# Performance work log

Measured on AMD Instinct MI355X. Metric: run time of the kernel, lower is better.

## Reference

```python
import jax, jax.numpy as jnp
import numpy as np

B_, L_, DM_, DS_, DC_, EXP_ = 2, 2048, 1024, 16, 4, 2
DI_ = EXP_ * DM_

def setup_inputs() -> dict:
    key = jax.random.key(0)
    ks = jax.random.split(key, 8)
    rn = lambda k, shape, s: (jax.random.normal(k, shape, dtype=jnp.float32) * s)
    return {
        "x": rn(ks[0], (B_, L_, DM_), 1.0),
        "in_proj_w": rn(ks[1], (2 * DI_, DM_), 0.02),
        "conv_w": rn(ks[2], (DI_, 1, DC_), 0.1),
        "conv_b": jnp.zeros((DI_,), dtype=jnp.float32),
        "x_proj_w": rn(ks[3], (2 * DS_ + 1, DI_), 0.02),
        "dt_proj_w": rn(ks[4], (DI_, 1), 0.02),
        "dt_proj_b": jnp.full((DI_,), -2.0, dtype=jnp.float32),
        "A_log": rn(ks[5], (DI_, DS_), 1.0),
        "D": jnp.ones((DI_,), dtype=jnp.float32),
        "out_proj_w": rn(ks[6], (DM_, DI_), 0.02),
    }


def reference(x, in_proj_w, conv_w, conv_b, x_proj_w, dt_proj_w, dt_proj_b, A_log, D, out_proj_w):
    b, l, dm = x.shape
    di, ds = A_log.shape
    dc = conv_w.shape[-1]

    # in_proj -> split into u (ssm stream) and z (gate)
    xz = x @ in_proj_w.T                      # (b, l, 2*di)
    u, z = xz[..., :di], xz[..., di:]

    # causal depthwise conv1d (torch pads both sides then slices [:l] == left pad only)
    uc = jnp.transpose(u, (0, 2, 1))          # (b, di, l)
    uc = jax.lax.conv_general_dilated(
        uc, conv_w, window_strides=(1,), padding=[(dc - 1, 0)],
        feature_group_count=di, dimension_numbers=("NCH", "OIH", "NCH"))
    uc = uc + conv_b[None, :, None]
    u = jnp.transpose(uc, (0, 2, 1)) * jax.nn.silu(z)   # (b, l, di)

    # input-dependent SSM params
    proj = u @ x_proj_w.T                     # (b, l, 2*ds + 1)
    delta = proj[..., :1]                     # (b, l, 1)
    Bm = proj[..., 1:1 + ds]                  # (b, l, ds)
    Cm = proj[..., 1 + ds:]                   # (b, l, ds)
    delta = jax.nn.softplus(delta @ dt_proj_w.T + dt_proj_b)  # (b, l, di)

    A = -jnp.exp(A_log)                       # (di, ds)

    def step(h, inp):
        ut, dt, Bt, Ct = inp                  # (b,di) (b,di) (b,ds) (b,ds)
        dte = jnp.exp(dt)                     # faithful to source: exp(softplus(...))
        A_bar = jnp.exp(A[None] * dte[..., None])          # (b, di, ds)
        h = A_bar * h + (Bt[:, None, :] * dte[..., None]) * ut[..., None]
        yt = jnp.einsum("bis,bs->bi", h, Ct) + D * ut
        return h, yt

    h0 = jnp.zeros((b, di, ds), dtype=x.dtype)
    xs = (jnp.transpose(u, (1, 0, 2)), jnp.transpose(delta, (1, 0, 2)),
          jnp.transpose(Bm, (1, 0, 2)), jnp.transpose(Cm, (1, 0, 2)))
    _, ys = jax.lax.scan(step, h0, xs)        # ys: (l, b, di)
    y = jnp.transpose(ys, (1, 0, 2))          # (b, l, di)
    return y @ out_proj_w.T                   # (b, l, dm)
```

## Files before the change

kernel.cpp:

```cpp
#include <hip/hip_runtime.h>
#include <hip/hip_bf16.h>
#include <cstddef>
#include <cstdint>

#define B_N 2
#define L_N 2048
#define DM_N 1024
#define DS_N 16
#define DI_N 2048
#define NTOK (B_N * L_N)
#define NPROJ 33
#define NPJ 36
#define NC 64
#define CL (L_N / NC)
#define XKC 8
#define XKCL (DI_N / XKC)

typedef __attribute__((ext_vector_type(8))) short short8v;
typedef __attribute__((ext_vector_type(4))) float f32x4;
typedef __attribute__((address_space(1))) void av1;
typedef __attribute__((address_space(3))) void av3;

__device__ __forceinline__ void gload16(const void* g, void* l) {
  __builtin_amdgcn_global_load_lds((av1*)g, (av3*)l, 16, 0, 0);
}

__device__ __forceinline__ unsigned short f2bf_rn(float f) {
  uint32_t u = __float_as_uint(f);
  uint32_t r = (u + 0x7fffu + ((u >> 16) & 1u)) >> 16;
  return (unsigned short)r;
}
__device__ __forceinline__ float bf2f(unsigned short h) {
  return __uint_as_float((uint32_t)h << 16);
}

__global__ __launch_bounds__(256) void split_pack_kernel(
    const float* __restrict__ src, uint32_t* __restrict__ dst, int n8) {
  int idx = blockIdx.x * 256 + threadIdx.x;
  if (idx >= n8) return;
  const float4* s = (const float4*)src + (size_t)idx * 2;
  float4 v0 = s[0], v1 = s[1];
  float f[8] = {v0.x, v0.y, v0.z, v0.w, v1.x, v1.y, v1.z, v1.w};
  uint32_t hi[4], lo[4];
#pragma unroll
  for (int j = 0; j < 4; ++j) {
    unsigned short h0 = f2bf_rn(f[2 * j]);
    unsigned short h1 = f2bf_rn(f[2 * j + 1]);
    unsigned short l0 = f2bf_rn(f[2 * j] - bf2f(h0));
    unsigned short l1 = f2bf_rn(f[2 * j + 1] - bf2f(h1));
    hi[j] = (uint32_t)h0 | ((uint32_t)h1 << 16);
    lo[j] = (uint32_t)l0 | ((uint32_t)l1 << 16);
  }
  uint4* d = (uint4*)dst + (size_t)idx * 2;
  d[0] = make_uint4(hi[0], hi[1], hi[2], hi[3]);
  d[1] = make_uint4(lo[0], lo[1], lo[2], lo[3]);
}

__global__ __launch_bounds__(256) void gemm_pk_nt(
    const char* __restrict__ Apk, const char* __restrict__ Bpk,
    float* __restrict__ C, int N, int K4, int gx) {
  __shared__ __align__(16) char lds[32768];
  const int tid = threadIdx.x;
  const int lane = tid & 63;
  const int wave = tid >> 6;

  const int nwg = gridDim.x;
  const int cpx = nwg >> 3;
  const int bid = blockIdx.x;
  const int wg = (bid & 7) * cpx + (bid >> 3);
  const int bx = wg % gx;
  const int by = wg / gx;
  const int m0 = by * 128, n0 = bx * 128;

  const int wr = wave >> 1, wc = wave & 1;

  const char* gbase = (wave & 2) ? Bpk : Apk;
  const int rowbase = ((wave & 2) ? n0 : m0) + (wave & 1) * 64;
  const int rloc = lane >> 3;
  const int sslot = (lane & 7) ^ rloc;
  const char* gsrc = gbase + (size_t)(rowbase + rloc) * K4 + sslot * 16;
  const size_t cstride = (size_t)8 * K4;
  char* ldst = lds + wave * 8192 + lane * 16;

  f32x4 acc[4][4] = {};
  const int fr = lane & 15;
  const int fg = lane >> 4;
  const int sA = ((fg * 2) ^ (fr & 7)) * 16;
  const int abase = (wr * 64 + fr) * 128 + sA;
  const int bbase = 16384 + (wc * 64 + fr) * 128 + sA;

  for (int kt4 = 0; kt4 < K4; kt4 += 128) {
#pragma unroll
    for (int c = 0; c < 8; ++c)
      gload16(gsrc + c * cstride + kt4, ldst + c * 1024);
    __syncthreads();

    short8v afh[4], afl[4], bfh[4], bfl[4];
#pragma unroll
    for (int m = 0; m < 4; ++m) {
      int a = abase + m * 2048;
      afh[m] = *(const short8v*)(lds + a);
      afl[m] = *(const short8v*)(lds + (a ^ 16));
    }
#pragma unroll
    for (int n = 0; n < 4; ++n) {
      int b = bbase + n * 2048;
      bfh[n] = *(const short8v*)(lds + b);
      bfl[n] = *(const short8v*)(lds + (b ^ 16));
    }
#pragma unroll
    for (int m = 0; m < 4; ++m) {
#pragma unroll
      for (int n = 0; n < 4; ++n) {
        asm("v_mfma_f32_16x16x32_bf16 %0, %1, %2, %0"
            : "+v"(acc[m][n]) : "v"(afh[m]), "v"(bfh[n]));
        asm("v_mfma_f32_16x16x32_bf16 %0, %1, %2, %0"
            : "+v"(acc[m][n]) : "v"(afh[m]), "v"(bfl[n]));
        asm("v_mfma_f32_16x16x32_bf16 %0, %1, %2, %0"
            : "+v"(acc[m][n]) : "v"(afl[m]), "v"(bfh[n]));
      }
    }
    __syncthreads();
  }

#pragma unroll
  for (int m = 0; m < 4; ++m) {
#pragma unroll
    for (int n = 0; n < 4; ++n) {
#pragma unroll
      for (int q = 0; q < 4; ++q) {
        int row = m0 + wr * 64 + m * 16 + fg * 4 + q;
        int col = n0 + wc * 64 + n * 16 + fr;
        C[(size_t)row * N + col] = acc[m][n][q];
      }
    }
  }
}

__global__ __launch_bounds__(256) void gemm2_pk_nt(
    const char* __restrict__ Apk, const char* __restrict__ Bpk,
    float* __restrict__ C) {
  __shared__ __align__(16) char lds[24576];
  const int tid = threadIdx.x;
  const int lane = tid & 63;
  const int wave = tid >> 6;
  const int K4 = DI_N * 4;

  const int bid = blockIdx.x;
  const int wg = (bid & 7) * 64 + (bid >> 3);
  const int bx = wg >> 6;
  const int by = wg & 63;
  const int m0 = by * 64, n0 = bx * 128;

  const int rloc = tid >> 3;
  const int sl = (tid & 7) ^ (rloc & 7);
  const char* gA = Apk + (size_t)(m0 + rloc) * K4 + sl * 16;
  const char* gB = Bpk + (size_t)(n0 + rloc) * K4 + sl * 16;
  const size_t cs = (size_t)32 * K4;
  char* ldst = lds + tid * 16;

  f32x4 acc[4][2] = {};
  const int fr = lane & 15;
  const int fg = lane >> 4;
  const int sA = ((fg * 2) ^ (fr & 7)) * 16;
  const int abase0 = fr * 128 + sA;
  const int bbase0 = 8192 + (wave * 32 + fr) * 128 + sA;

  for (int kt4 = 0; kt4 < K4; kt4 += 128) {
    gload16(gA + kt4, ldst);
    gload16(gA + cs + kt4, ldst + 4096);
    gload16(gB + kt4, ldst + 8192);
    gload16(gB + cs + kt4, ldst + 12288);
    gload16(gB + 2 * cs + kt4, ldst + 16384);
    gload16(gB + 3 * cs + kt4, ldst + 20480);
    __syncthreads();

    short8v afh[4], afl[4], bfh[2], bfl[2];
#pragma unroll
    for (int m = 0; m < 4; ++m) {
      int a = abase0 + m * 2048;
      afh[m] = *(const short8v*)(lds + a);
      afl[m] = *(const short8v*)(lds + (a ^ 16));
    }
#pragma unroll
    for (int n = 0; n < 2; ++n) {
      int b = bbase0 + n * 2048;
      bfh[n] = *(const short8v*)(lds + b);
      bfl[n] = *(const short8v*)(lds + (b ^ 16));
    }
#pragma unroll
    for (int m = 0; m < 4; ++m) {
#pragma unroll
      for (int n = 0; n < 2; ++n) {
        asm("v_mfma_f32_16x16x32_bf16 %0, %1, %2, %0"
            : "+v"(acc[m][n]) : "v"(afh[m]), "v"(bfh[n]));
        asm("v_mfma_f32_16x16x32_bf16 %0, %1, %2, %0"
            : "+v"(acc[m][n]) : "v"(afh[m]), "v"(bfl[n]));
        asm("v_mfma_f32_16x16x32_bf16 %0, %1, %2, %0"
            : "+v"(acc[m][n]) : "v"(afl[m]), "v"(bfh[n]));
      }
    }
    __syncthreads();
  }

#pragma unroll
  for (int m = 0; m < 4; ++m) {
#pragma unroll
    for (int n = 0; n < 2; ++n) {
#pragma unroll
      for (int q = 0; q < 4; ++q) {
        int row = m0 + m * 16 + fg * 4 + q;
        int col = n0 + wave * 32 + n * 16 + fr;
        C[(size_t)row * DM_N + col] = acc[m][n][q];
      }
    }
  }
}

__global__ __launch_bounds__(256) void conv_silu_kernel(
    const float* __restrict__ xz, const float* __restrict__ cw,
    const float* __restrict__ cb, float* __restrict__ u2) {
  int idx = blockIdx.x * 256 + threadIdx.x;
  int i4 = idx & (DI_N / 4 - 1);
  int n = idx >> 9;
  int i = i4 << 2;
  int l = n & (L_N - 1);
  const float* base = xz + (size_t)n * (2 * DI_N) + i;
  float4 zero = {0.f, 0.f, 0.f, 0.f};
  float4 u0 = *(const float4*)base;
  float4 u1 = (l >= 1) ? *(const float4*)(base - 2 * DI_N) : zero;
  float4 um2 = (l >= 2) ? *(const float4*)(base - 4 * DI_N) : zero;
  float4 um3 = (l >= 3) ? *(const float4*)(base - 6 * DI_N) : zero;
  float4 z = *(const float4*)(base + DI_N);
  float4 bia = *(const float4*)&cb[i];
  float4 w0 = *(const float4*)&cw[i * 4];
  float4 w1 = *(const float4*)&cw[i * 4 + 4];
  float4 w2 = *(const float4*)&cw[i * 4 + 8];
  float4 w3 = *(const float4*)&cw[i * 4 + 12];
  float4 r;
  r.x = fmaf(w0.w, u0.x, fmaf(w0.z, u1.x, fmaf(w0.y, um2.x, fmaf(w0.x, um3.x, bia.x))));
  r.y = fmaf(w1.w, u0.y, fmaf(w1.z, u1.y, fmaf(w1.y, um2.y, fmaf(w1.x, um3.y, bia.y))));
  r.z = fmaf(w2.w, u0.z, fmaf(w2.z, u1.z, fmaf(w2.y, um2.z, fmaf(w2.x, um3.z, bia.z))));
  r.w = fmaf(w3.w, u0.w, fmaf(w3.z, u1.w, fmaf(w3.y, um2.w, fmaf(w3.x, um3.w, bia.w))));
  r.x *= z.x / (1.f + __expf(-z.x));
  r.y *= z.y / (1.f + __expf(-z.y));
  r.z *= z.z / (1.f + __expf(-z.z));
  r.w *= z.w / (1.f + __expf(-z.w));
  *(float4*)&u2[(size_t)n * DI_N + i] = r;
}

__global__ __launch_bounds__(256) void xproj_part_kernel(
    const float* __restrict__ u2, const float* __restrict__ xw,
    float* __restrict__ part) {
  __shared__ float uS[16][257];
  __shared__ float wS[33][257];
  const int tid = threadIdx.x;
  const int kc = blockIdx.x & (XKC - 1);
  const int rb = blockIdx.x >> 3;
  const int row0 = rb * 16;
  const int k0 = kc * XKCL;

#pragma unroll
  for (int it = 0; it < 4; ++it) {
    int slot = tid + it * 256;
    int r = slot >> 6;
    int kq = (slot & 63) << 2;
    float4 v = *(const float4*)&u2[(size_t)(row0 + r) * DI_N + k0 + kq];
    uS[r][kq] = v.x; uS[r][kq + 1] = v.y;
    uS[r][kq + 2] = v.z; uS[r][kq + 3] = v.w;
  }
#pragma unroll
  for (int it = 0; it < 9; ++it) {
    int slot = tid + it * 256;
    if (slot < 33 * 64) {
      int c = slot >> 6;
      int kq = (slot & 63) << 2;
      float4 v = *(const float4*)&xw[(size_t)c * DI_N + k0 + kq];
      wS[c][kq] = v.x; wS[c][kq + 1] = v.y;
      wS[c][kq + 2] = v.z; wS[c][kq + 3] = v.w;
    }
  }
  __syncthreads();

  const int r = tid & 15;
  const int cg = tid >> 4;
  const int c0 = cg * 3;
  const int rc0 = c0 > 32 ? 32 : c0;
  const int rc1 = c0 + 1 > 32 ? 32 : c0 + 1;
  const int rc2 = c0 + 2 > 32 ? 32 : c0 + 2;
  float a0 = 0.f, a1 = 0.f, a2 = 0.f;
#pragma unroll 4
  for (int k = 0; k < XKCL; ++k) {
    float uv = uS[r][k];
    a0 = fmaf(uv, wS[rc0][k], a0);
    a1 = fmaf(uv, wS[rc1][k], a1);
    a2 = fmaf(uv, wS[rc2][k], a2);
  }
  size_t base = (size_t)kc * (NTOK * NPJ) + (size_t)(row0 + r) * NPJ;
  if (c0 < NPROJ)     part[base + (c0 == 0 ? 0 : c0 + 3)] = a0;
  if (c0 + 1 < NPROJ) part[base + c0 + 4] = a1;
  if (c0 + 2 < NPROJ) part[base + c0 + 5] = a2;
  if (cg == 11) {
    part[base + 1] = 0.f; part[base + 2] = 0.f; part[base + 3] = 0.f;
  }
}

__global__ __launch_bounds__(256) void xproj_reduce_kernel(
    const float* __restrict__ part, float* __restrict__ proj) {
  int idx = blockIdx.x * 256 + threadIdx.x;
  float s = 0.f;
#pragma unroll
  for (int kc = 0; kc < XKC; ++kc)
    s += part[(size_t)kc * (NTOK * NPJ) + idx];
  proj[idx] = s;
}

__global__ __launch_bounds__(256) void scan_pass1_kernel(
    const float* __restrict__ u2, const float* __restrict__ pj,
    const float* __restrict__ dtw, const float* __restrict__ dtb,
    const float* __restrict__ A_log,
    float* __restrict__ carryH, float* __restrict__ sdteO) {
  __shared__ float pS[CL][20];
  const int tid = threadIdx.x;
  const int bid = blockIdx.x;
  const int ib = bid & 7;
  const int c = (bid >> 3) & (NC - 1);
  const int b = bid >> 9;
  const int i = ib * 256 + tid;
  const int l0 = c * CL;
  const float LOG2E = 1.4426950408889634f;

  if (tid < CL * 5) {
    int row = tid / 5, j = tid % 5;
    float4 v = *(const float4*)&pj[((size_t)b * L_N + l0 + row) * NPJ + j * 4];
    *(float4*)&pS[row][j * 4] = v;
  }

  float A2[16];
#pragma unroll
  for (int q = 0; q < 4; ++q) {
    float4 v = *(const float4*)&A_log[i * DS_N + q * 4];
    A2[q * 4 + 0] = -__expf(v.x) * LOG2E;
    A2[q * 4 + 1] = -__expf(v.y) * LOG2E;
    A2[q * 4 + 2] = -__expf(v.z) * LOG2E;
    A2[q * 4 + 3] = -__expf(v.w) * LOG2E;
  }
  const float wl = dtw[i] * LOG2E;
  const float bl = dtb[i] * LOG2E;
  const float* un = u2 + ((size_t)b * L_N + l0) * DI_N + i;
  __syncthreads();

  float h[16] = {};
  float sdte = 0.f;
  float ucur = un[0];
#pragma unroll 2
  for (int l = 0; l < CL; ++l) {
    float unext = (l + 1 < CL) ? un[(size_t)(l + 1) * DI_N] : 0.f;
    float d0 = pS[l][0];
    float4 B0 = *(const float4*)&pS[l][4];
    float4 B1 = *(const float4*)&pS[l][8];
    float4 B2 = *(const float4*)&pS[l][12];
    float4 B3 = *(const float4*)&pS[l][16];
    float dte = 1.f + exp2f(fmaf(d0, wl, bl));
    float du = dte * ucur;
    sdte += dte;
    float Bv[16] = {B0.x, B0.y, B0.z, B0.w, B1.x, B1.y, B1.z, B1.w,
                    B2.x, B2.y, B2.z, B2.w, B3.x, B3.y, B3.z, B3.w};
#pragma unroll
    for (int s = 0; s < 16; ++s) {
      float a = exp2f(A2[s] * dte);
      h[s] = fmaf(a, h[s], Bv[s] * du);
    }
    ucur = unext;
  }
  size_t cbase = (((size_t)c * B_N + b) * DI_N + i) * DS_N;
#pragma unroll
  for (int q = 0; q < 4; ++q) {
    float4 hv = {h[q * 4], h[q * 4 + 1], h[q * 4 + 2], h[q * 4 + 3]};
    *(float4*)&carryH[cbase + q * 4] = hv;
  }
  sdteO[((size_t)c * B_N + b) * DI_N + i] = sdte;
}

__global__ __launch_bounds__(256) void scan_fixup_kernel(
    float* __restrict__ carryH, const float* __restrict__ sdte,
    const float* __restrict__ A_log) {
  const int q = blockIdx.x * 256 + threadIdx.x;
  const int s = q & 15;
  const int i = (q >> 4) & (DI_N - 1);
  const float LOG2E = 1.4426950408889634f;
  const float A2 = -__expf(A_log[i * DS_N + s]) * LOG2E;
  float h = 0.f;
#pragma unroll 8
  for (int c = 0; c < NC; ++c) {
    size_t idx = (size_t)c * (B_N * DI_N * DS_N) + q;
    float Hc = carryH[idx];
    float sd = sdte[(size_t)c * (B_N * DI_N) + (q >> 4)];
    carryH[idx] = h;
    h = fmaf(exp2f(A2 * sd), h, Hc);
  }
}

__global__ __launch_bounds__(256) void scan_pass2_kernel(
    const float* __restrict__ u2, const float* __restrict__ pj,
    const float* __restrict__ dtw, const float* __restrict__ dtb,
    const float* __restrict__ A_log, const float* __restrict__ Dp,
    const float* __restrict__ carryH, char* __restrict__ ypk) {
  __shared__ float pS[CL][36];
  const int tid = threadIdx.x;
  const int bid = blockIdx.x;
  const int ib = bid & 7;
  const int c = (bid >> 3) & (NC - 1);
  const int b = bid >> 9;
  const int i = ib * 256 + tid;
  const int l0 = c * CL;
  const float LOG2E = 1.4426950408889634f;

#pragma unroll
  for (int it = 0; it < 2; ++it) {
    int slot = tid + it * 256;
    if (slot < CL * 9) {
      int row = slot / 9, j = slot % 9;
      float4 v = *(const float4*)&pj[((size_t)b * L_N + l0 + row) * NPJ + j * 4];
      *(float4*)&pS[row][j * 4] = v;
    }
  }

  float A2[16];
#pragma unroll
  for (int q = 0; q < 4; ++q) {
    float4 v = *(const float4*)&A_log[i * DS_N + q * 4];
    A2[q * 4 + 0] = -__expf(v.x) * LOG2E;
    A2[q * 4 + 1] = -__expf(v.y) * LOG2E;
    A2[q * 4 + 2] = -__expf(v.z) * LOG2E;
    A2[q * 4 + 3] = -__expf(v.w) * LOG2E;
  }
  const float wl = dtw[i] * LOG2E;
  const float bl = dtb[i] * LOG2E;
  const float Dd = Dp[i];

  float h[16];
  size_t cbase = (((size_t)c * B_N + b) * DI_N + i) * DS_N;
#pragma unroll
  for (int q = 0; q < 4; ++q) {
    float4 hv = *(const float4*)&carryH[cbase + q * 4];
    h[q * 4] = hv.x; h[q * 4 + 1] = hv.y;
    h[q * 4 + 2] = hv.z; h[q * 4 + 3] = hv.w;
  }

  const float* un = u2 + ((size_t)b * L_N + l0) * DI_N + i;
  char* yb = ypk + ((size_t)b * L_N + l0) * (DI_N * 4) + (i >> 3) * 32 + (i & 7) * 2;
  __syncthreads();

  float ucur = un[0];
#pragma unroll 2
  for (int l = 0; l < CL; ++l) {
    float unext = (l + 1 < CL) ? un[(size_t)(l + 1) * DI_N] : 0.f;
    float d0 = pS[l][0];
    float4 B0 = *(const float4*)&pS[l][4];
    float4 B1 = *(const float4*)&pS[l][8];
    float4 B2 = *(const float4*)&pS[l][12];
    float4 B3 = *(const float4*)&pS[l][16];
    float4 C0 = *(const float4*)&pS[l][20];
    float4 C1 = *(const float4*)&pS[l][24];
    float4 C2 = *(const float4*)&pS[l][28];
    float4 C3 = *(const float4*)&pS[l][32];
    float dte = 1.f + exp2f(fmaf(d0, wl, bl));
    float du = dte * ucur;
    float Bv[16] = {B0.x, B0.y, B0.z, B0.w, B1.x, B1.y, B1.z, B1.w,
                    B2.x, B2.y, B2.z, B2.w, B3.x, B3.y, B3.z, B3.w};
    float Cv[16] = {C0.x, C0.y, C0.z, C0.w, C1.x, C1.y, C1.z, C1.w,
                    C2.x, C2.y, C2.z, C2.w, C3.x, C3.y, C3.z, C3.w};
    float y = Dd * ucur;
#pragma unroll
    for (int s = 0; s < 16; ++s) {
      float a = exp2f(A2[s] * dte);
      h[s] = fmaf(a, h[s], Bv[s] * du);
      y = fmaf(h[s], Cv[s], y);
    }
    unsigned short hh = f2bf_rn(y);
    char* q = yb + (size_t)l * (DI_N * 4);
    *(unsigned short*)q = hh;
    *(unsigned short*)(q + 16) = f2bf_rn(y - bf2f(hh));
    ucur = unext;
  }
}

extern "C" void kernel_launch(void* const* d_in, const int* in_sizes, int n_in,
                              void* d_out, int out_size, void* d_ws, size_t ws_size,
                              hipStream_t stream) {
  const float* x          = (const float*)d_in[0];
  const float* in_proj_w  = (const float*)d_in[1];
  const float* conv_w     = (const float*)d_in[2];
  const float* conv_b     = (const float*)d_in[3];
  const float* x_proj_w   = (const float*)d_in[4];
  const float* dt_proj_w  = (const float*)d_in[5];
  const float* dt_proj_b  = (const float*)d_in[6];
  const float* A_log      = (const float*)d_in[7];
  const float* Dp         = (const float*)d_in[8];
  const float* out_proj_w = (const float*)d_in[9];
  float* out = (float*)d_out;

  char* ws = (char*)d_ws;
  float* xz = (float*)ws;
  float* u2 = (float*)(ws + (size_t)NTOK * 2 * DI_N * 4);

  char* x_pk  = (char*)u2;
  char* w1_pk = x_pk + (size_t)NTOK * DM_N * 4;

  char*  y_pk   = ws;
  float* carryH = (float*)(ws + 33554432);
  float* sdte   = (float*)(ws + 50331648);
  char*  w2_pk  = ws + 51380224;
  float* xpart  = (float*)(ws + 59768832);
  float* proj36 = (float*)(ws + 64487424);

  {
    int n8 = NTOK * DM_N / 8;
    split_pack_kernel<<<n8 / 256, 256, 0, stream>>>(x, (uint32_t*)x_pk, n8);
    split_pack_kernel<<<n8 / 256, 256, 0, stream>>>(in_proj_w, (uint32_t*)w1_pk, n8);
  }
  gemm_pk_nt<<<1024, 256, 0, stream>>>(x_pk, w1_pk, xz, 2 * DI_N, DM_N * 4, 32);
  conv_silu_kernel<<<(NTOK * DI_N / 4) / 256, 256, 0, stream>>>(xz, conv_w,
                                                                conv_b, u2);
  {
    int n8 = DM_N * DI_N / 8;
    split_pack_kernel<<<n8 / 256, 256, 0, stream>>>(out_proj_w, (uint32_t*)w2_pk, n8);
  }
  {
    xproj_part_kernel<<<(NTOK / 16) * XKC, 256, 0, stream>>>(u2, x_proj_w, xpart);
    xproj_reduce_kernel<<<(NTOK * NPJ) / 256, 256, 0, stream>>>(xpart, proj36);
  }
  {
    int nblk = B_N * NC * (DI_N / 256);
    scan_pass1_kernel<<<nblk, 256, 0, stream>>>(u2, proj36, dt_proj_w, dt_proj_b,
                                                A_log, carryH, sdte);
    scan_fixup_kernel<<<(B_N * DI_N * DS_N) / 256, 256, 0, stream>>>(carryH, sdte,
                                                                     A_log);
    scan_pass2_kernel<<<nblk, 256, 0, stream>>>(u2, proj36, dt_proj_w, dt_proj_b,
                                                A_log, Dp, carryH, y_pk);
  }
  gemm2_pk_nt<<<512, 256, 0, stream>>>(y_pk, w2_pk, out);
}
```

Before: 354.7 us.

## Pre-swizzle packed bf16 operands in global memory for contiguous LDS loads

The split/pack kernel and the scan's y output now write the hi/lo bf16 chunks directly in the XOR-swizzled order the GEMM LDS layout expects, with an extra row-bit term in the swizzle. The GEMM global loads then read contiguous 16-byte slots without per-lane XOR, which is meant to improve coalescing of the direct-to-LDS loads and reduce LDS bank conflicts. Separately, the conv/SiLU kernel processes 8 channels per thread instead of 4, halving the thread count. The producer and consumer layouts must match exactly, so correctness depends on the swizzle formulas agreeing across three kernels.

```diff
diff --git a/kernel.cpp b/kernel.cpp
--- a/kernel.cpp
+++ b/kernel.cpp
@@ -35,9 +35,15 @@
 }
 
 __global__ __launch_bounds__(256) void split_pack_kernel(
-    const float* __restrict__ src, uint32_t* __restrict__ dst, int n8) {
+    const float* __restrict__ src, char* __restrict__ dst, int n8, int gshift) {
   int idx = blockIdx.x * 256 + threadIdx.x;
   if (idx >= n8) return;
+  int row = idx >> gshift;
+  int g = idx & ((1 << gshift) - 1);
+  int x = (row & 7) ^ ((row >> 3) & 1);
+  int gl2 = (g & 3) * 2;
+  size_t base = ((size_t)row << (gshift + 5)) + (size_t)(g >> 2) * 128;
+
   const float4* s = (const float4*)src + (size_t)idx * 2;
   float4 v0 = s[0], v1 = s[1];
   float f[8] = {v0.x, v0.y, v0.z, v0.w, v1.x, v1.y, v1.z, v1.w};
@@ -51,9 +57,10 @@
     hi[j] = (uint32_t)h0 | ((uint32_t)h1 << 16);
     lo[j] = (uint32_t)l0 | ((uint32_t)l1 << 16);
   }
-  uint4* d = (uint4*)dst + (size_t)idx * 2;
-  d[0] = make_uint4(hi[0], hi[1], hi[2], hi[3]);
-  d[1] = make_uint4(lo[0], lo[1], lo[2], lo[3]);
+  *(uint4*)(dst + base + (size_t)((gl2 ^ x) << 4)) =
+      make_uint4(hi[0], hi[1], hi[2], hi[3]);
+  *(uint4*)(dst + base + (size_t)(((gl2 + 1) ^ x) << 4)) =
+      make_uint4(lo[0], lo[1], lo[2], lo[3]);
 }
 
 __global__ __launch_bounds__(256) void gemm_pk_nt(
@@ -77,15 +84,14 @@
   const char* gbase = (wave & 2) ? Bpk : Apk;
   const int rowbase = ((wave & 2) ? n0 : m0) + (wave & 1) * 64;
   const int rloc = lane >> 3;
-  const int sslot = (lane & 7) ^ rloc;
-  const char* gsrc = gbase + (size_t)(rowbase + rloc) * K4 + sslot * 16;
+  const char* gsrc = gbase + (size_t)(rowbase + rloc) * K4 + (lane & 7) * 16;
   const size_t cstride = (size_t)8 * K4;
   char* ldst = lds + wave * 8192 + lane * 16;
 
   f32x4 acc[4][4] = {};
   const int fr = lane & 15;
   const int fg = lane >> 4;
-  const int sA = ((fg * 2) ^ (fr & 7)) * 16;
+  const int sA = ((fg * 2) ^ (fr & 7) ^ ((fr >> 3) & 1)) * 16;
   const int abase = (wr * 64 + fr) * 128 + sA;
   const int bbase = 16384 + (wc * 64 + fr) * 128 + sA;
 
@@ -153,16 +159,15 @@
   const int m0 = by * 64, n0 = bx * 128;
 
   const int rloc = tid >> 3;
-  const int sl = (tid & 7) ^ (rloc & 7);
-  const char* gA = Apk + (size_t)(m0 + rloc) * K4 + sl * 16;
-  const char* gB = Bpk + (size_t)(n0 + rloc) * K4 + sl * 16;
+  const char* gA = Apk + (size_t)(m0 + rloc) * K4 + (tid & 7) * 16;
+  const char* gB = Bpk + (size_t)(n0 + rloc) * K4 + (tid & 7) * 16;
   const size_t cs = (size_t)32 * K4;
   char* ldst = lds + tid * 16;
 
   f32x4 acc[4][2] = {};
   const int fr = lane & 15;
   const int fg = lane >> 4;
-  const int sA = ((fg * 2) ^ (fr & 7)) * 16;
+  const int sA = ((fg * 2) ^ (fr & 7) ^ ((fr >> 3) & 1)) * 16;
   const int abase0 = fr * 128 + sA;
   const int bbase0 = 8192 + (wave * 32 + fr) * 128 + sA;
 
@@ -221,32 +226,37 @@
     const float* __restrict__ xz, const float* __restrict__ cw,
     const float* __restrict__ cb, float* __restrict__ u2) {
   int idx = blockIdx.x * 256 + threadIdx.x;
-  int i4 = idx & (DI_N / 4 - 1);
-  int n = idx >> 9;
-  int i = i4 << 2;
+  int i8 = idx & (DI_N / 8 - 1);
+  int n = idx >> 8;
+  int i0 = i8 << 3;
   int l = n & (L_N - 1);
-  const float* base = xz + (size_t)n * (2 * DI_N) + i;
-  float4 zero = {0.f, 0.f, 0.f, 0.f};
-  float4 u0 = *(const float4*)base;
-  float4 u1 = (l >= 1) ? *(const float4*)(base - 2 * DI_N) : zero;
-  float4 um2 = (l >= 2) ? *(const float4*)(base - 4 * DI_N) : zero;
-  float4 um3 = (l >= 3) ? *(const float4*)(base - 6 * DI_N) : zero;
-  float4 z = *(const float4*)(base + DI_N);
-  float4 bia = *(const float4*)&cb[i];
-  float4 w0 = *(const float4*)&cw[i * 4];
-  float4 w1 = *(const float4*)&cw[i * 4 + 4];
-  float4 w2 = *(const float4*)&cw[i * 4 + 8];
-  float4 w3 = *(const float4*)&cw[i * 4 + 12];
-  float4 r;
-  r.x = fmaf(w0.w, u0.x, fmaf(w0.z, u1.x, fmaf(w0.y, um2.x, fmaf(w0.x, um3.x, bia.x))));
-  r.y = fmaf(w1.w, u0.y, fmaf(w1.z, u1.y, fmaf(w1.y, um2.y, fmaf(w1.x, um3.y, bia.y))));
-  r.z = fmaf(w2.w, u0.z, fmaf(w2.z, u1.z, fmaf(w2.y, um2.z, fmaf(w2.x, um3.z, bia.z))));
-  r.w = fmaf(w3.w, u0.w, fmaf(w3.z, u1.w, fmaf(w3.y, um2.w, fmaf(w3.x, um3.w, bia.w))));
-  r.x *= z.x / (1.f + __expf(-z.x));
-  r.y *= z.y / (1.f + __expf(-z.y));
-  r.z *= z.z / (1.f + __expf(-z.z));
-  r.w *= z.w / (1.f + __expf(-z.w));
-  *(float4*)&u2[(size_t)n * DI_N + i] = r;
+  const float* rowbase = xz + (size_t)n * (2 * DI_N);
+#pragma unroll
+  for (int h = 0; h < 2; ++h) {
+    int i = i0 + h * 4;
+    const float* base = rowbase + i;
+    float4 zero = {0.f, 0.f, 0.f, 0.f};
+    float4 u0 = *(const float4*)base;
+    float4 u1 = (l >= 1) ? *(const float4*)(base - 2 * DI_N) : zero;
+    float4 um2 = (l >= 2) ? *(const float4*)(base - 4 * DI_N) : zero;
+    float4 um3 = (l >= 3) ? *(const float4*)(base - 6 * DI_N) : zero;
+    float4 z = *(const float4*)(base + DI_N);
+    float4 bia = *(const float4*)&cb[i];
+    float4 w0 = *(const float4*)&cw[i * 4];
+    float4 w1 = *(const float4*)&cw[i * 4 + 4];
+    float4 w2 = *(const float4*)&cw[i * 4 + 8];
+    float4 w3 = *(const float4*)&cw[i * 4 + 12];
+    float4 r;
+    r.x = fmaf(w0.w, u0.x, fmaf(w0.z, u1.x, fmaf(w0.y, um2.x, fmaf(w0.x, um3.x, bia.x))));
+    r.y = fmaf(w1.w, u0.y, fmaf(w1.z, u1.y, fmaf(w1.y, um2.y, fmaf(w1.x, um3.y, bia.y))));
+    r.z = fmaf(w2.w, u0.z, fmaf(w2.z, u1.z, fmaf(w2.y, um2.z, fmaf(w2.x, um3.z, bia.z))));
+    r.w = fmaf(w3.w, u0.w, fmaf(w3.z, u1.w, fmaf(w3.y, um2.w, fmaf(w3.x, um3.w, bia.w))));
+    r.x *= z.x / (1.f + __expf(-z.x));
+    r.y *= z.y / (1.f + __expf(-z.y));
+    r.z *= z.z / (1.f + __expf(-z.z));
+    r.w *= z.w / (1.f + __expf(-z.w));
+    *(float4*)&u2[(size_t)n * DI_N + i] = r;
+  }
 }
 
 __global__ __launch_bounds__(256) void xproj_part_kernel(
@@ -449,7 +459,10 @@
   }
 
   const float* un = u2 + ((size_t)b * L_N + l0) * DI_N + i;
-  char* yb = ypk + ((size_t)b * L_N + l0) * (DI_N * 4) + (i >> 3) * 32 + (i & 7) * 2;
+  const int g = i >> 3;
+  const int gl2 = (g & 3) * 2;
+  char* yrow = ypk + ((size_t)b * L_N + l0) * (DI_N * 4) + (g >> 2) * 128
+             + (i & 7) * 2;
   __syncthreads();
 
   float ucur = un[0];
@@ -479,9 +492,10 @@
       y = fmaf(h[s], Cv[s], y);
     }
     unsigned short hh = f2bf_rn(y);
-    char* q = yb + (size_t)l * (DI_N * 4);
-    *(unsigned short*)q = hh;
-    *(unsigned short*)(q + 16) = f2bf_rn(y - bf2f(hh));
+    int x = (l & 7) ^ ((l >> 3) & 1);
+    char* q = yrow + (size_t)l * (DI_N * 4);
+    *(unsigned short*)(q + ((gl2 ^ x) << 4)) = hh;
+    *(unsigned short*)(q + (((gl2 + 1) ^ x) << 4)) = f2bf_rn(y - bf2f(hh));
     ucur = unext;
   }
 }
@@ -517,15 +531,15 @@
 
   {
     int n8 = NTOK * DM_N / 8;
-    split_pack_kernel<<<n8 / 256, 256, 0, stream>>>(x, (uint32_t*)x_pk, n8);
-    split_pack_kernel<<<n8 / 256, 256, 0, stream>>>(in_proj_w, (uint32_t*)w1_pk, n8);
+    split_pack_kernel<<<n8 / 256, 256, 0, stream>>>(x, x_pk, n8, 7);
+    split_pack_kernel<<<n8 / 256, 256, 0, stream>>>(in_proj_w, w1_pk, n8, 7);
   }
   gemm_pk_nt<<<1024, 256, 0, stream>>>(x_pk, w1_pk, xz, 2 * DI_N, DM_N * 4, 32);
-  conv_silu_kernel<<<(NTOK * DI_N / 4) / 256, 256, 0, stream>>>(xz, conv_w,
+  conv_silu_kernel<<<(NTOK * DI_N / 8) / 256, 256, 0, stream>>>(xz, conv_w,
                                                                 conv_b, u2);
   {
     int n8 = DM_N * DI_N / 8;
-    split_pack_kernel<<<n8 / 256, 256, 0, stream>>>(out_proj_w, (uint32_t*)w2_pk, n8);
+    split_pack_kernel<<<n8 / 256, 256, 0, stream>>>(out_proj_w, w2_pk, n8, 8);
   }
   {
     xproj_part_kernel<<<(NTOK / 16) * XKC, 256, 0, stream>>>(u2, x_proj_w, xpart);
```

New measurement: 392.4 us. 10.6% more time.
